# Kernel tuning notes

Hardware: AMD Instinct MI355X
Metric: run time of the kernel (lower is better)

Reference implementation:

```python
import jax, jax.numpy as jnp
import numpy as np
from jax import lax

B, T, IN, H, OUT = 4096, 512, 2, 12, 2


def setup_inputs() -> dict:
    key = jax.random.key(0)
    ks = jax.random.split(key, 11)
    s = 1.0 / np.sqrt(H)  # PyTorch LSTM init scale
    f32 = jnp.float32
    return {
        "x": jax.random.normal(ks[0], (B, T, IN), dtype=f32),
        "W_ih0": jax.random.uniform(ks[1], (4 * H, IN), dtype=f32, minval=-s, maxval=s),
        "W_hh0": jax.random.uniform(ks[2], (4 * H, H), dtype=f32, minval=-s, maxval=s),
        "b_ih0": jax.random.uniform(ks[3], (4 * H,), dtype=f32, minval=-s, maxval=s),
        "b_hh0": jax.random.uniform(ks[4], (4 * H,), dtype=f32, minval=-s, maxval=s),
        "W_ih1": jax.random.uniform(ks[5], (4 * H, H), dtype=f32, minval=-s, maxval=s),
        "W_hh1": jax.random.uniform(ks[6], (4 * H, H), dtype=f32, minval=-s, maxval=s),
        "b_ih1": jax.random.uniform(ks[7], (4 * H,), dtype=f32, minval=-s, maxval=s),
        "b_hh1": jax.random.uniform(ks[8], (4 * H,), dtype=f32, minval=-s, maxval=s),
        "fc_W": jax.random.uniform(ks[9], (OUT, H), dtype=f32, minval=-s, maxval=s),
        "fc_b": jax.random.uniform(ks[10], (OUT,), dtype=f32, minval=-s, maxval=s),
    }


def _lstm_layer(x, W_ih, W_hh, b_ih, b_hh):
    # x: [B, T, in_dim] -> hidden trajectory [B, T, H]
    b, h = x.shape[0], W_hh.shape[1]
    # Precompute input contribution for all timesteps: [T, B, 4H]
    xg = jnp.einsum('bti,gi->tbg', x, W_ih) + b_ih + b_hh

    def step(carry, xg_t):
        hprev, cprev = carry
        gates = xg_t + hprev @ W_hh.T  # [B, 4H], PyTorch gate order i,f,g,o
        i, f, g, o = jnp.split(gates, 4, axis=-1)
        i = jax.nn.sigmoid(i)
        f = jax.nn.sigmoid(f)
        g = jnp.tanh(g)
        o = jax.nn.sigmoid(o)
        c = f * cprev + i * g
        hnew = o * jnp.tanh(c)
        return (hnew, c), hnew

    z = jnp.zeros((b, h), dtype=x.dtype)
    _, hs = lax.scan(step, (z, z), xg)  # hs: [T, B, H]
    return jnp.swapaxes(hs, 0, 1)  # [B, T, H]


def reference(x, W_ih0, W_hh0, b_ih0, b_hh0, W_ih1, W_hh1, b_ih1, b_hh1, fc_W, fc_b):
    # 2-layer LSTM, h0=c0=0; dropout is identity in eval mode.
    h1 = _lstm_layer(x, W_ih0, W_hh0, b_ih0, b_hh0)   # [B, T, H]
    h2 = _lstm_layer(h1, W_ih1, W_hh1, b_ih1, b_hh1)  # [B, T, H]
    last = h2[:, -1, :]                               # [B, H]
    return last @ fc_W.T + fc_b                       # [B, OUT]
```

## Files before the change

### kernel.cpp

```cpp
#include <hip/hip_runtime.h>


namespace {
constexpr int H  = 12;
constexpr int T  = 512;
constexpr int IN = 2;

__device__ __forceinline__ float rcp_(float v) { return __builtin_amdgcn_rcpf(v); }
__device__ __forceinline__ float sigm_(float v) { return rcp_(1.0f + __expf(-v)); }
__device__ __forceinline__ float tanh_(float v) {
    return fmaf(-2.0f, rcp_(1.0f + __expf(2.0f * v)), 1.0f);
}
__device__ __forceinline__ float bperm_(int addr, float v) {
    return __int_as_float(__builtin_amdgcn_ds_bpermute(addr, __float_as_int(v)));
}
}

__global__ __launch_bounds__(256, 1) void lstm2_fc_kernel(
    const float* __restrict__ x,
    const float* __restrict__ W_ih0,
    const float* __restrict__ W_hh0,
    const float* __restrict__ b_ih0,
    const float* __restrict__ b_hh0,
    const float* __restrict__ W_ih1,
    const float* __restrict__ W_hh1,
    const float* __restrict__ b_ih1,
    const float* __restrict__ b_hh1,
    const float* __restrict__ fc_W,
    const float* __restrict__ fc_b,
    float* __restrict__ out)
{
    const int tid  = threadIdx.x;
    const int lane = tid & 63;
    const int u    = tid & 15;
    const int grp  = tid >> 4;
    const int b    = blockIdx.x * 16 + grp;
    const int uc   = (u < H) ? u : 0;

    const int pbase = (lane & 48) << 2;

    float wih0[4][IN], whh0[4][H], wih1[4][H], whh1[4][H];
    float bias0[4], bias1[4];
#pragma unroll
    for (int g = 0; g < 4; ++g) {
        const int r = g * H + uc;
        bias0[g] = b_ih0[r] + b_hh0[r];
        bias1[g] = b_ih1[r] + b_hh1[r];
        wih0[g][0] = W_ih0[r * IN + 0];
        wih0[g][1] = W_ih0[r * IN + 1];
#pragma unroll
        for (int j = 0; j < H; ++j) {
            whh0[g][j] = W_hh0[r * H + j];
            wih1[g][j] = W_ih1[r * H + j];
            whh1[g][j] = W_hh1[r * H + j];
        }
    }

    float c0 = 0.0f, c1 = 0.0f;
    float h0b[H], h1b[H];
#pragma unroll
    for (int j = 0; j < H; ++j) { h0b[j] = 0.0f; h1b[j] = 0.0f; }

    const float* xb = x + (size_t)b * T * IN;
    float2 xc = *(const float2*)xb;

    for (int t = 0; t < T; ++t) {
        const int tn = (t < T - 1) ? (t + 1) : t;
        const float2 xn = *(const float2*)(xb + tn * IN);

        float a0[4];
#pragma unroll
        for (int g = 0; g < 4; ++g) {
            float acc = fmaf(wih0[g][0], xc.x, bias0[g]);
            acc = fmaf(wih0[g][1], xc.y, acc);
#pragma unroll
            for (int j = 0; j < H; ++j) acc = fmaf(whh0[g][j], h0b[j], acc);
            a0[g] = acc;
        }
        {
            const float i0 = sigm_(a0[0]);
            const float f0 = sigm_(a0[1]);
            const float g0 = tanh_(a0[2]);
            const float o0 = sigm_(a0[3]);
            c0 = fmaf(f0, c0, i0 * g0);
            const float h0 = o0 * tanh_(c0);
#pragma unroll
            for (int j = 0; j < H; ++j) h0b[j] = bperm_(pbase + 4 * j, h0);
        }

        float a1[4];
#pragma unroll
        for (int g = 0; g < 4; ++g) {
            float acc = bias1[g];
#pragma unroll
            for (int j = 0; j < H; ++j) acc = fmaf(whh1[g][j], h1b[j], acc);
#pragma unroll
            for (int j = 0; j < H; ++j) acc = fmaf(wih1[g][j], h0b[j], acc);
            a1[g] = acc;
        }
        {
            const float i1 = sigm_(a1[0]);
            const float f1 = sigm_(a1[1]);
            const float g1 = tanh_(a1[2]);
            const float o1 = sigm_(a1[3]);
            c1 = fmaf(f1, c1, i1 * g1);
            const float h1 = o1 * tanh_(c1);
#pragma unroll
            for (int j = 0; j < H; ++j) h1b[j] = bperm_(pbase + 4 * j, h1);
        }

        xc = xn;
    }

    if (u == 0) {
        float r0 = fc_b[0];
        float r1 = fc_b[1];
#pragma unroll
        for (int j = 0; j < H; ++j) {
            r0 = fmaf(fc_W[j],      h1b[j], r0);
            r1 = fmaf(fc_W[H + j],  h1b[j], r1);
        }
        float2 res; res.x = r0; res.y = r1;
        *(float2*)(out + (size_t)b * 2) = res;
    }
}

extern "C" void kernel_launch(void* const* d_in, const int* in_sizes, int n_in,
                              void* d_out, int out_size, void* d_ws, size_t ws_size,
                              hipStream_t stream) {
    const float* x     = (const float*)d_in[0];
    const float* W_ih0 = (const float*)d_in[1];
    const float* W_hh0 = (const float*)d_in[2];
    const float* b_ih0 = (const float*)d_in[3];
    const float* b_hh0 = (const float*)d_in[4];
    const float* W_ih1 = (const float*)d_in[5];
    const float* W_hh1 = (const float*)d_in[6];
    const float* b_ih1 = (const float*)d_in[7];
    const float* b_hh1 = (const float*)d_in[8];
    const float* fc_W  = (const float*)d_in[9];
    const float* fc_b  = (const float*)d_in[10];
    float* out = (float*)d_out;

    lstm2_fc_kernel<<<256, 256, 0, stream>>>(
        x, W_ih0, W_hh0, b_ih0, b_hh0,
        W_ih1, W_hh1, b_ih1, b_hh1, fc_W, fc_b, out);
}
```

Baseline: 314.1 us.

## Split LSTM gates across two half-groups and use ds_swizzle broadcasts

Each batch row now gets 32 lanes instead of 16. Each lane computes two of the four gate pre-activations, and the g/o gate values are exchanged between the halves with an XOR-16 swizzle. The tanh gate reuses the sigmoid through a 2*sigm(2x)-1 affine trick. The hidden-state broadcast changes from address-based ds_bpermute to immediate-pattern ds_swizzle, and the launch doubles to 512 blocks with launch bounds allowing 2 blocks per CU. This halves per-lane FMA and register work on the serial recurrence critical path, at the cost of twice the lanes and extra cross-lane exchanges.

After: 276.2 us. 12.1% less time.

```diff
diff --git a/kernel.cpp b/kernel.cpp
--- a/kernel.cpp
+++ b/kernel.cpp
@@ -11,12 +11,25 @@
 __device__ __forceinline__ float tanh_(float v) {
     return fmaf(-2.0f, rcp_(1.0f + __expf(2.0f * v)), 1.0f);
 }
-__device__ __forceinline__ float bperm_(int addr, float v) {
-    return __int_as_float(__builtin_amdgcn_ds_bpermute(addr, __float_as_int(v)));
+template <int IMM>
+__device__ __forceinline__ float swzf(float v) {
+    return __int_as_float(__builtin_amdgcn_ds_swizzle(__float_as_int(v), IMM));
 }
 }
 
-__global__ __launch_bounds__(256, 1) void lstm2_fc_kernel(
+#define BC12(dst, v)                                                         \
+    do {                                                                     \
+        dst[0]  = swzf<(0 << 5)>(v);  dst[1]  = swzf<(1 << 5)>(v);           \
+        dst[2]  = swzf<(2 << 5)>(v);  dst[3]  = swzf<(3 << 5)>(v);           \
+        dst[4]  = swzf<(4 << 5)>(v);  dst[5]  = swzf<(5 << 5)>(v);           \
+        dst[6]  = swzf<(6 << 5)>(v);  dst[7]  = swzf<(7 << 5)>(v);           \
+        dst[8]  = swzf<(8 << 5)>(v);  dst[9]  = swzf<(9 << 5)>(v);           \
+        dst[10] = swzf<(10 << 5)>(v); dst[11] = swzf<(11 << 5)>(v);          \
+    } while (0)
+
+#define XOR16 0x401F
+
+__global__ __launch_bounds__(256, 2) void lstm2_fc_kernel(
     const float* __restrict__ x,
     const float* __restrict__ W_ih0,
     const float* __restrict__ W_hh0,
@@ -31,30 +44,33 @@
     float* __restrict__ out)
 {
     const int tid  = threadIdx.x;
-    const int lane = tid & 63;
-    const int u    = tid & 15;
-    const int grp  = tid >> 4;
-    const int b    = blockIdx.x * 16 + grp;
+    const int p    = tid & 31;
+    const int u    = p & 15;
+    const int half = p >> 4;
+    const int b    = blockIdx.x * 8 + (tid >> 5);
     const int uc   = (u < H) ? u : 0;
 
-    const int pbase = (lane & 48) << 2;
+    const int rA = (2 * half) * H + uc;
+    const int rB = rA + H;
 
-    float wih0[4][IN], whh0[4][H], wih1[4][H], whh1[4][H];
-    float bias0[4], bias1[4];
+    const float preA = half ? 2.0f : 1.0f;
+    const float pmA  = half ? 2.0f : 1.0f;
+    const float paA  = half ? -1.0f : 0.0f;
+
+    float wih0A[IN], wih0B[IN];
+    float whh0A[H], whh0B[H], wih1A[H], wih1B[H], whh1A[H], whh1B[H];
+    wih0A[0] = W_ih0[rA * IN + 0]; wih0A[1] = W_ih0[rA * IN + 1];
+    wih0B[0] = W_ih0[rB * IN + 0]; wih0B[1] = W_ih0[rB * IN + 1];
 #pragma unroll
-    for (int g = 0; g < 4; ++g) {
-        const int r = g * H + uc;
-        bias0[g] = b_ih0[r] + b_hh0[r];
-        bias1[g] = b_ih1[r] + b_hh1[r];
-        wih0[g][0] = W_ih0[r * IN + 0];
-        wih0[g][1] = W_ih0[r * IN + 1];
-#pragma unroll
-        for (int j = 0; j < H; ++j) {
-            whh0[g][j] = W_hh0[r * H + j];
-            wih1[g][j] = W_ih1[r * H + j];
-            whh1[g][j] = W_hh1[r * H + j];
-        }
+    for (int j = 0; j < H; ++j) {
+        whh0A[j] = W_hh0[rA * H + j];  whh0B[j] = W_hh0[rB * H + j];
+        wih1A[j] = W_ih1[rA * H + j];  wih1B[j] = W_ih1[rB * H + j];
+        whh1A[j] = W_hh1[rA * H + j];  whh1B[j] = W_hh1[rB * H + j];
     }
+    const float biasA0 = b_ih0[rA] + b_hh0[rA];
+    const float biasB0 = b_ih0[rB] + b_hh0[rB];
+    const float biasA1 = b_ih1[rA] + b_hh1[rA];
+    const float biasB1 = b_ih1[rB] + b_hh1[rB];
 
     float c0 = 0.0f, c1 = 0.0f;
     float h0b[H], h1b[H];
@@ -68,57 +84,52 @@
         const int tn = (t < T - 1) ? (t + 1) : t;
         const float2 xn = *(const float2*)(xb + tn * IN);
 
-        float a0[4];
+        float aA = fmaf(wih0A[0], xc.x, biasA0);
+        float aB = fmaf(wih0B[0], xc.x, biasB0);
+        aA = fmaf(wih0A[1], xc.y, aA);
+        aB = fmaf(wih0B[1], xc.y, aB);
 #pragma unroll
-        for (int g = 0; g < 4; ++g) {
-            float acc = fmaf(wih0[g][0], xc.x, bias0[g]);
-            acc = fmaf(wih0[g][1], xc.y, acc);
+        for (int j = 0; j < H; ++j) {
+            aA = fmaf(whh0A[j], h0b[j], aA);
+            aB = fmaf(whh0B[j], h0b[j], aB);
+        }
+        const float sA0 = fmaf(pmA, sigm_(preA * aA), paA);
+        const float sB0 = sigm_(aB);
+        const float gv0 = swzf<XOR16>(sA0);
+        const float ov0 = swzf<XOR16>(sB0);
+        c0 = fmaf(sB0, c0, sA0 * gv0);
+        const float h0 = ov0 * tanh_(c0);
+        BC12(h0b, h0);
+
+        float a1A = biasA1, a1B = biasB1;
 #pragma unroll
-            for (int j = 0; j < H; ++j) acc = fmaf(whh0[g][j], h0b[j], acc);
-            a0[g] = acc;
+        for (int j = 0; j < H; ++j) {
+            a1A = fmaf(whh1A[j], h1b[j], a1A);
+            a1B = fmaf(whh1B[j], h1b[j], a1B);
         }
-        {
-            const float i0 = sigm_(a0[0]);
-            const float f0 = sigm_(a0[1]);
-            const float g0 = tanh_(a0[2]);
-            const float o0 = sigm_(a0[3]);
-            c0 = fmaf(f0, c0, i0 * g0);
-            const float h0 = o0 * tanh_(c0);
 #pragma unroll
-            for (int j = 0; j < H; ++j) h0b[j] = bperm_(pbase + 4 * j, h0);
+        for (int j = 0; j < H; ++j) {
+            a1A = fmaf(wih1A[j], h0b[j], a1A);
+            a1B = fmaf(wih1B[j], h0b[j], a1B);
         }
-
-        float a1[4];
-#pragma unroll
-        for (int g = 0; g < 4; ++g) {
-            float acc = bias1[g];
-#pragma unroll
-            for (int j = 0; j < H; ++j) acc = fmaf(whh1[g][j], h1b[j], acc);
-#pragma unroll
-            for (int j = 0; j < H; ++j) acc = fmaf(wih1[g][j], h0b[j], acc);
-            a1[g] = acc;
-        }
-        {
-            const float i1 = sigm_(a1[0]);
-            const float f1 = sigm_(a1[1]);
-            const float g1 = tanh_(a1[2]);
-            const float o1 = sigm_(a1[3]);
-            c1 = fmaf(f1, c1, i1 * g1);
-            const float h1 = o1 * tanh_(c1);
-#pragma unroll
-            for (int j = 0; j < H; ++j) h1b[j] = bperm_(pbase + 4 * j, h1);
-        }
+        const float sA1 = fmaf(pmA, sigm_(preA * a1A), paA);
+        const float sB1 = sigm_(a1B);
+        const float gv1 = swzf<XOR16>(sA1);
+        const float ov1 = swzf<XOR16>(sB1);
+        c1 = fmaf(sB1, c1, sA1 * gv1);
+        const float h1 = ov1 * tanh_(c1);
+        BC12(h1b, h1);
 
         xc = xn;
     }
 
-    if (u == 0) {
+    if (p == 0) {
         float r0 = fc_b[0];
         float r1 = fc_b[1];
 #pragma unroll
         for (int j = 0; j < H; ++j) {
-            r0 = fmaf(fc_W[j],      h1b[j], r0);
-            r1 = fmaf(fc_W[H + j],  h1b[j], r1);
+            r0 = fmaf(fc_W[j],     h1b[j], r0);
+            r1 = fmaf(fc_W[H + j], h1b[j], r1);
         }
         float2 res; res.x = r0; res.y = r1;
         *(float2*)(out + (size_t)b * 2) = res;
@@ -141,7 +152,7 @@
     const float* fc_b  = (const float*)d_in[10];
     float* out = (float*)d_out;
 
-    lstm2_fc_kernel<<<256, 256, 0, stream>>>(
+    lstm2_fc_kernel<<<512, 256, 0, stream>>>(
         x, W_ih0, W_hh0, b_ih0, b_hh0,
         W_ih1, W_hh1, b_ih1, b_hh1, fc_W, fc_b, out);
 }
```

## Map one batch per wavefront with one gate row per lane

Applied to the files above, without the earlier changes.

Each wavefront now handles a single batch element, with each lane owning one gate row (unit×4+gate). That cuts the per-thread FMA chain per step roughly fourfold, and the launch grows to 1024 blocks at 4 blocks per CU. Gate values are exchanged between neighbouring lanes with DPP quad permutes, and hidden states are broadcast with readlane instead of ds_bpermute. A single fused sigmoid/tanh path built on a raw v_exp_f32 replaces the separate helpers. This raises total VALU work and leaves many lanes idle, in exchange for shorter serial latency per timestep and more waves per SIMD to hide it.

After: 324.0 us. 3.2% more time.

```diff
diff --git a/kernel.cpp b/kernel.cpp
--- a/kernel.cpp
+++ b/kernel.cpp
@@ -5,18 +5,33 @@
 constexpr int H  = 12;
 constexpr int T  = 512;
 constexpr int IN = 2;
+constexpr float LOG2E = 1.4426950408889634f;
 
-__device__ __forceinline__ float rcp_(float v) { return __builtin_amdgcn_rcpf(v); }
-__device__ __forceinline__ float sigm_(float v) { return rcp_(1.0f + __expf(-v)); }
-__device__ __forceinline__ float tanh_(float v) {
-    return fmaf(-2.0f, rcp_(1.0f + __expf(2.0f * v)), 1.0f);
+__device__ __forceinline__ float exp2_(float x) {
+    float r;
+    asm("v_exp_f32 %0, %1" : "=v"(r) : "v"(x));
+    return r;
 }
-__device__ __forceinline__ float bperm_(int addr, float v) {
-    return __int_as_float(__builtin_amdgcn_ds_bpermute(addr, __float_as_int(v)));
+__device__ __forceinline__ float rcp_(float x) { return __builtin_amdgcn_rcpf(x); }
+
+template <int CTRL>
+__device__ __forceinline__ float dppf(float v) {
+    return __int_as_float(__builtin_amdgcn_update_dpp(
+        __float_as_int(v), __float_as_int(v), CTRL, 0xF, 0xF, true));
+}
+constexpr int QP1 = 0x39;
+constexpr int QP2 = 0x4E;
+constexpr int QP3 = 0x93;
+
+__device__ __forceinline__ float rdl(float v, int l) {
+    return __int_as_float(__builtin_amdgcn_readlane(__float_as_int(v), l));
+}
+__device__ __forceinline__ float tanh_(float c) {
+    return fmaf(2.0f, rcp_(1.0f + exp2_(-2.0f * LOG2E * c)), -1.0f);
 }
 }
 
-__global__ __launch_bounds__(256, 1) void lstm2_fc_kernel(
+__global__ __launch_bounds__(256, 4) void lstm2_fc_kernel(
     const float* __restrict__ x,
     const float* __restrict__ W_ih0,
     const float* __restrict__ W_hh0,
@@ -30,95 +45,92 @@
     const float* __restrict__ fc_b,
     float* __restrict__ out)
 {
-    const int tid  = threadIdx.x;
-    const int lane = tid & 63;
-    const int u    = tid & 15;
-    const int grp  = tid >> 4;
-    const int b    = blockIdx.x * 16 + grp;
+    const int lane = threadIdx.x & 63;
+    const int wid  = __builtin_amdgcn_readfirstlane((int)threadIdx.x >> 6);
+    const int b    = blockIdx.x * 4 + wid;
+    const int u    = lane >> 2;
+    const int gate = lane & 3;
     const int uc   = (u < H) ? u : 0;
+    const int r    = gate * H + uc;
 
-    const int pbase = (lane & 48) << 2;
+    const float pre  = (gate == 2) ? 2.0f : 1.0f;
+    const float kmul = -LOG2E * pre;
+    const float pa   = 1.0f - pre;
 
-    float wih0[4][IN], whh0[4][H], wih1[4][H], whh1[4][H];
-    float bias0[4], bias1[4];
+    const float wx0 = W_ih0[r * IN + 0];
+    const float wx1 = W_ih0[r * IN + 1];
+    float whh0[H], wih1[H], whh1[H];
 #pragma unroll
-    for (int g = 0; g < 4; ++g) {
-        const int r = g * H + uc;
-        bias0[g] = b_ih0[r] + b_hh0[r];
-        bias1[g] = b_ih1[r] + b_hh1[r];
-        wih0[g][0] = W_ih0[r * IN + 0];
-        wih0[g][1] = W_ih0[r * IN + 1];
-#pragma unroll
-        for (int j = 0; j < H; ++j) {
-            whh0[g][j] = W_hh0[r * H + j];
-            wih1[g][j] = W_ih1[r * H + j];
-            whh1[g][j] = W_hh1[r * H + j];
-        }
+    for (int j = 0; j < H; ++j) {
+        whh0[j] = W_hh0[r * H + j];
+        wih1[j] = W_ih1[r * H + j];
+        whh1[j] = W_hh1[r * H + j];
     }
+    const float bias0 = b_ih0[r] + b_hh0[r];
+    const float bias1 = b_ih1[r] + b_hh1[r];
 
     float c0 = 0.0f, c1 = 0.0f;
-    float h0b[H], h1b[H];
+    float h0s[H], h1s[H];
 #pragma unroll
-    for (int j = 0; j < H; ++j) { h0b[j] = 0.0f; h1b[j] = 0.0f; }
+    for (int j = 0; j < H; ++j) { h0s[j] = 0.0f; h1s[j] = 0.0f; }
 
-    const float* xb = x + (size_t)b * T * IN;
-    float2 xc = *(const float2*)xb;
+    const float* xp = x + (size_t)b * T * IN;
+    float xv0 = xp[0], xv1 = xp[1];
 
     for (int t = 0; t < T; ++t) {
         const int tn = (t < T - 1) ? (t + 1) : t;
-        const float2 xn = *(const float2*)(xb + tn * IN);
+        const float xn0 = xp[2 * tn + 0];
+        const float xn1 = xp[2 * tn + 1];
 
-        float a0[4];
+        float aA = fmaf(wx0, xv0, bias0);
+        aA = fmaf(wx1, xv1, aA);
+        float aB = whh0[0] * h0s[0];
 #pragma unroll
-        for (int g = 0; g < 4; ++g) {
-            float acc = fmaf(wih0[g][0], xc.x, bias0[g]);
-            acc = fmaf(wih0[g][1], xc.y, acc);
+        for (int j = 1; j < 6; ++j) aB = fmaf(whh0[j], h0s[j], aB);
 #pragma unroll
-            for (int j = 0; j < H; ++j) acc = fmaf(whh0[g][j], h0b[j], acc);
-            a0[g] = acc;
-        }
-        {
-            const float i0 = sigm_(a0[0]);
-            const float f0 = sigm_(a0[1]);
-            const float g0 = tanh_(a0[2]);
-            const float o0 = sigm_(a0[3]);
-            c0 = fmaf(f0, c0, i0 * g0);
-            const float h0 = o0 * tanh_(c0);
+        for (int j = 6; j < H; ++j) aA = fmaf(whh0[j], h0s[j], aA);
+        const float a0 = aA + aB;
+
+        const float s0 = fmaf(pre, rcp_(1.0f + exp2_(kmul * a0)), pa);
+        const float f0 = dppf<QP1>(s0);
+        const float g0 = dppf<QP2>(s0);
+        const float o0 = dppf<QP3>(s0);
+        c0 = fmaf(f0, c0, s0 * g0);
+        const float h0v = o0 * tanh_(c0);
 #pragma unroll
-            for (int j = 0; j < H; ++j) h0b[j] = bperm_(pbase + 4 * j, h0);
-        }
+        for (int j = 0; j < H; ++j) h0s[j] = rdl(h0v, 4 * j);
 
-        float a1[4];
+        float bA = bias1;
 #pragma unroll
-        for (int g = 0; g < 4; ++g) {
-            float acc = bias1[g];
+        for (int j = 0; j < 6; ++j) bA = fmaf(whh1[j], h1s[j], bA);
+        float bB = whh1[6] * h1s[6];
 #pragma unroll
-            for (int j = 0; j < H; ++j) acc = fmaf(whh1[g][j], h1b[j], acc);
+        for (int j = 7; j < H; ++j) bB = fmaf(whh1[j], h1s[j], bB);
 #pragma unroll
-            for (int j = 0; j < H; ++j) acc = fmaf(wih1[g][j], h0b[j], acc);
-            a1[g] = acc;
-        }
-        {
-            const float i1 = sigm_(a1[0]);
-            const float f1 = sigm_(a1[1]);
-            const float g1 = tanh_(a1[2]);
-            const float o1 = sigm_(a1[3]);
-            c1 = fmaf(f1, c1, i1 * g1);
-            const float h1 = o1 * tanh_(c1);
+        for (int j = 0; j < 6; ++j) bA = fmaf(wih1[j], h0s[j], bA);
 #pragma unroll
-            for (int j = 0; j < H; ++j) h1b[j] = bperm_(pbase + 4 * j, h1);
-        }
+        for (int j = 6; j < H; ++j) bB = fmaf(wih1[j], h0s[j], bB);
+        const float a1 = bA + bB;
 
-        xc = xn;
+        const float s1 = fmaf(pre, rcp_(1.0f + exp2_(kmul * a1)), pa);
+        const float f1 = dppf<QP1>(s1);
+        const float g1 = dppf<QP2>(s1);
+        const float o1 = dppf<QP3>(s1);
+        c1 = fmaf(f1, c1, s1 * g1);
+        const float h1v = o1 * tanh_(c1);
+#pragma unroll
+        for (int j = 0; j < H; ++j) h1s[j] = rdl(h1v, 4 * j);
+
+        xv0 = xn0; xv1 = xn1;
     }
 
-    if (u == 0) {
+    if (lane == 0) {
         float r0 = fc_b[0];
         float r1 = fc_b[1];
 #pragma unroll
         for (int j = 0; j < H; ++j) {
-            r0 = fmaf(fc_W[j],      h1b[j], r0);
-            r1 = fmaf(fc_W[H + j],  h1b[j], r1);
+            r0 = fmaf(fc_W[j],     h1s[j], r0);
+            r1 = fmaf(fc_W[H + j], h1s[j], r1);
         }
         float2 res; res.x = r0; res.y = r1;
         *(float2*)(out + (size_t)b * 2) = res;
@@ -141,7 +153,7 @@
     const float* fc_b  = (const float*)d_in[10];
     float* out = (float*)d_out;
 
-    lstm2_fc_kernel<<<256, 256, 0, stream>>>(
+    lstm2_fc_kernel<<<1024, 256, 0, stream>>>(
         x, W_ih0, W_hh0, b_ih0, b_hh0,
         W_ih1, W_hh1, b_ih1, b_hh1, fc_W, fc_b, out);
 }
```
